# Kernel optimization log

Hardware: AMD Instinct MI355X
Metric: run time of the kernel (lower is better)

Reference implementation:

```python
import jax, jax.numpy as jnp
import numpy as np

D = 1024
H = 16
DK = D // H
TB = 64  # temporal_bias_dim
SCALE = DK ** -0.5


def setup_inputs() -> dict:
    key = jax.random.key(0)
    ks = jax.random.split(key, 12)
    B, S = 8, 512
    s = 0.02
    return {
        "x": jax.random.normal(ks[0], (B, S, D), jnp.float32),
        "padding_masks": jnp.ones((B, 1, 1, S), jnp.int32),
        "batch_temporal_mat": jax.random.uniform(ks[1], (B, S, S), jnp.float32) * 100.0,
        "wq": jax.random.normal(ks[2], (D, D), jnp.float32) * s,
        "bq": jnp.zeros((D,), jnp.float32),
        "wk": jax.random.normal(ks[3], (D, D), jnp.float32) * s,
        "bk": jnp.zeros((D,), jnp.float32),
        "wv": jax.random.normal(ks[4], (D, D), jnp.float32) * s,
        "bv": jnp.zeros((D,), jnp.float32),
        "w_proj": jax.random.normal(ks[5], (D, D), jnp.float32) * s,
        "b_proj": jnp.zeros((D,), jnp.float32),
        "w_tb1": jax.random.normal(ks[6], (1, TB), jnp.float32) * 0.5,
        "b_tb1": jnp.zeros((TB,), jnp.float32),
        "w_tb2": jax.random.normal(ks[7], (TB, 1), jnp.float32) * 0.5,
        "b_tb2": jnp.zeros((1,), jnp.float32),
    }


def reference(x, padding_masks, batch_temporal_mat, wq, bq, wk, bk, wv, bv,
              w_proj, b_proj, w_tb1, b_tb1, w_tb2, b_tb2):
    B, S, _ = x.shape

    def heads(w, b):
        return (x @ w + b).reshape(B, S, H, DK).transpose(0, 2, 1, 3)  # (B,H,S,DK)

    q, k, v = heads(wq, bq), heads(wk, bk), heads(wv, bv)
    scores = jnp.einsum("bhqd,bhkd->bhqk", q, k) * SCALE  # (B,H,S,S)

    # temporal bias: 1/log(e + t) -> Linear(1,64) -> leaky_relu(0.2) -> Linear(64,1)
    t = 1.0 / jnp.log(jnp.exp(jnp.float32(1.0)) + batch_temporal_mat)  # (B,S,S)
    h = t[..., None] * w_tb1[0] + b_tb1  # (B,S,S,TB)
    h = jnp.where(h >= 0, h, 0.2 * h)
    bias = (h @ w_tb2)[..., 0] + b_tb2[0]  # (B,S,S)
    scores = scores + bias[:, None, :, :]

    neg_inf = jnp.float32(-jnp.inf)
    scores = jnp.where(padding_masks == 0, neg_inf, scores)
    causal = jnp.triu(jnp.ones((S, S), bool), k=1)  # (S,S), add_cls=False
    scores = jnp.where(causal[None, None], neg_inf, scores)

    p_attn = jax.nn.softmax(scores, axis=-1)
    out = jnp.einsum("bhqk,bhkd->bhqd", p_attn, v)
    out = out.transpose(0, 2, 1, 3).reshape(B, S, D)
    out = out @ w_proj + b_proj
    return out
```

## Files before the change

### kernel.cpp

```cpp
#include <hip/hip_runtime.h>
#include <hip/hip_bf16.h>

#define B_  8
#define S_  512
#define D_  1024
#define H_  16
#define DK_ 64
#define TB_ 64
#define SCALE_ 0.125f

typedef __attribute__((ext_vector_type(8))) short          bh8;
typedef __attribute__((ext_vector_type(4))) float          f32x4;
typedef __attribute__((ext_vector_type(8))) unsigned short us8;

__device__ __forceinline__ unsigned short f2bf(float f) {
    unsigned u = __float_as_uint(f);
    unsigned r = 0x7fffu + ((u >> 16) & 1u);
    return (unsigned short)((u + r) >> 16);
}
__device__ __forceinline__ float bf2f(unsigned short u) {
    return __uint_as_float((unsigned)u << 16);
}

__device__ __forceinline__ void gl16(const unsigned short* g, unsigned short* l) {
    __builtin_amdgcn_global_load_lds(
        (const __attribute__((address_space(1))) void*)g,
        (__attribute__((address_space(3))) void*)l, 16, 0, 0);
}

__global__ __launch_bounds__(256)
void cvt_x_kernel(const float* __restrict__ in, unsigned short* __restrict__ out, int n8)
{
    int i = blockIdx.x * 256 + threadIdx.x;
    if (i >= n8) return;
    float4 a = *(const float4*)&in[(size_t)i * 8];
    float4 b = *(const float4*)&in[(size_t)i * 8 + 4];
    us8 o;
    o[0] = f2bf(a.x); o[1] = f2bf(a.y); o[2] = f2bf(a.z); o[3] = f2bf(a.w);
    o[4] = f2bf(b.x); o[5] = f2bf(b.y); o[6] = f2bf(b.z); o[7] = f2bf(b.w);
    *(us8*)&out[(size_t)i * 8] = o;
}

__global__ __launch_bounds__(256)
void cvt_wt4_kernel(const float* __restrict__ w0, const float* __restrict__ w1,
                    const float* __restrict__ w2, const float* __restrict__ w3,
                    unsigned short* __restrict__ o0, unsigned short* __restrict__ o1,
                    unsigned short* __restrict__ o2, unsigned short* __restrict__ o3)
{
    __shared__ float t[64][65];
    const int z = blockIdx.z;
    const float* W = (z == 0) ? w0 : (z == 1) ? w1 : (z == 2) ? w2 : w3;
    unsigned short* Wt = (z == 0) ? o0 : (z == 1) ? o1 : (z == 2) ? o2 : o3;
    const int bx = blockIdx.x, by = blockIdx.y;
    const int c  = threadIdx.x & 63;
    const int r0 = threadIdx.x >> 6;
    #pragma unroll
    for (int i = 0; i < 16; ++i) {
        int r = r0 + i * 4;
        t[r][c] = W[(size_t)(by * 64 + r) * 1024 + bx * 64 + c];
    }
    __syncthreads();
    #pragma unroll
    for (int i = 0; i < 16; ++i) {
        int r = r0 + i * 4;
        Wt[(size_t)(bx * 64 + r) * 1024 + by * 64 + c] = f2bf(t[c][r]);
    }
}

__global__ __launch_bounds__(256)
void gemm_qkv_kernel(const unsigned short* __restrict__ A,
                     const unsigned short* __restrict__ Wt,
                     const float* __restrict__ bq, const float* __restrict__ bk,
                     const float* __restrict__ bv,
                     unsigned short* __restrict__ qo,
                     unsigned short* __restrict__ ko,
                     unsigned short* __restrict__ vo)
{
    __shared__ unsigned short As[128 * 64];
    __shared__ unsigned short Bs[64 * 64];
    const int tid  = threadIdx.x;
    const int lane = tid & 63;
    const int wid  = tid >> 6;
    const int wr   = wid >> 1, wc = wid & 1;
    const int row0 = blockIdx.x * 128;
    const int col0 = blockIdx.y * 64;

    f32x4 acc[4][2] = {};

    const int fr = lane & 15;
    const int g  = lane >> 4;
    const int sr = lane >> 3;
    const int sc = ((lane & 7) ^ sr) * 8;

    for (int k0 = 0; k0 < 1024; k0 += 64) {
        #pragma unroll
        for (int i = 0; i < 4; ++i)
            gl16(&A [(size_t)(row0 + wid * 32 + i * 8 + sr) * 1024 + k0 + sc],
                 &As[(wid * 32 + i * 8) * 64]);
        #pragma unroll
        for (int i = 0; i < 2; ++i)
            gl16(&Wt[(size_t)(col0 + wid * 16 + i * 8 + sr) * 1024 + k0 + sc],
                 &Bs[(wid * 16 + i * 8) * 64]);
        __syncthreads();
        #pragma unroll
        for (int ks = 0; ks < 2; ++ks) {
            const int ch = (ks * 4 + g) ^ (fr & 7);
            bh8 af[4], bfr[2];
            #pragma unroll
            for (int r = 0; r < 4; ++r)
                af[r]  = *(const bh8*)&As[(wr * 64 + r * 16 + fr) * 64 + ch * 8];
            #pragma unroll
            for (int c = 0; c < 2; ++c)
                bfr[c] = *(const bh8*)&Bs[(wc * 32 + c * 16 + fr) * 64 + ch * 8];
            #pragma unroll
            for (int r = 0; r < 4; ++r)
                #pragma unroll
                for (int c = 0; c < 2; ++c)
                    acc[r][c] = __builtin_amdgcn_mfma_f32_16x16x32_bf16(
                        af[r], bfr[c], acc[r][c], 0, 0, 0);
        }
        __syncthreads();
    }

    const int nh = col0 >> 10;
    const float* bsel = (nh == 0) ? bq : (nh == 1) ? bk : bv;
    unsigned short* outp = (nh == 0) ? qo : (nh == 1) ? ko : vo;

    #pragma unroll
    for (int r = 0; r < 4; ++r) {
        #pragma unroll
        for (int c = 0; c < 2; ++c) {
            int n  = col0 + wc * 32 + c * 16 + fr;
            int nn = n & 1023;
            float bn = bsel[nn];
            int hh = nn >> 6, dd = nn & 63;
            #pragma unroll
            for (int j = 0; j < 4; ++j) {
                int m = row0 + wr * 64 + r * 16 + g * 4 + j;
                float o = acc[r][c][j] + bn;
                int bb = m >> 9, ss = m & 511;
                if (nh == 2)
                    outp[((size_t)((bb * H_ + hh) * DK_ + dd)) * S_ + ss] = f2bf(o);
                else
                    outp[((size_t)((bb * H_ + hh) * S_ + ss)) * DK_ + dd] = f2bf(o);
            }
        }
    }
}

#define GEMM_STAGE(buf, k0) do {                                         \
    gl16(Arow + (k0),            &As[buf][(w * 16    ) * 64]);           \
    gl16(Arow + (k0) + 8 * 1024, &As[buf][(w * 16 + 8) * 64]);           \
    gl16(Brow + (k0),            &Bs[buf][(w * 16    ) * 64]);           \
    gl16(Brow + (k0) + 8 * 1024, &Bs[buf][(w * 16 + 8) * 64]);           \
} while (0)

#define GEMM_COMPUTE(buf) do {                                           \
    _Pragma("unroll")                                                    \
    for (int ks = 0; ks < 2; ++ks) {                                     \
        const int ch = (ks * 4 + g) ^ (fr & 7);                          \
        bh8 af[2], bf[2];                                                \
        _Pragma("unroll")                                                \
        for (int r = 0; r < 2; ++r)                                      \
            af[r] = *(const bh8*)&As[buf][(wr * 32 + r * 16 + fr) * 64 + ch * 8]; \
        _Pragma("unroll")                                                \
        for (int c = 0; c < 2; ++c)                                      \
            bf[c] = *(const bh8*)&Bs[buf][(wc * 32 + c * 16 + fr) * 64 + ch * 8]; \
        _Pragma("unroll")                                                \
        for (int r = 0; r < 2; ++r)                                      \
            _Pragma("unroll")                                            \
            for (int c = 0; c < 2; ++c)                                  \
                acc[r][c] = __builtin_amdgcn_mfma_f32_16x16x32_bf16(     \
                    af[r], bf[c], acc[r][c], 0, 0, 0);                   \
    }                                                                    \
} while (0)

__global__ __launch_bounds__(256)
void gemm_proj_kernel(const unsigned short* __restrict__ A,
                      const unsigned short* __restrict__ Wt,
                      const float* __restrict__ bias,
                      float* __restrict__ C)
{
    __shared__ unsigned short As[2][64 * 64];
    __shared__ unsigned short Bs[2][64 * 64];
    const int tid  = threadIdx.x;
    const int lane = tid & 63;
    const int w    = tid >> 6;
    const int wr   = w >> 1, wc = w & 1;
    const int row0 = blockIdx.x * 64;
    const int col0 = blockIdx.y * 64;

    f32x4 acc[2][2] = {};
    const int fr = lane & 15;
    const int g  = lane >> 4;
    const int sr = lane >> 3;
    const int sc = ((lane & 7) ^ sr) * 8;

    const unsigned short* Arow = A  + (size_t)(row0 + w * 16 + sr) * 1024 + sc;
    const unsigned short* Brow = Wt + (size_t)(col0 + w * 16 + sr) * 1024 + sc;

    GEMM_STAGE(0, 0);
    __syncthreads();
    int cur = 0;
    #pragma unroll 1
    for (int t = 0; t < 15; ++t) {
        GEMM_STAGE(cur ^ 1, (t + 1) * 64);
        GEMM_COMPUTE(cur);
        __syncthreads();
        cur ^= 1;
    }
    GEMM_COMPUTE(cur);

    #pragma unroll
    for (int r = 0; r < 2; ++r) {
        #pragma unroll
        for (int c = 0; c < 2; ++c) {
            int n = col0 + wc * 32 + c * 16 + fr;
            float bn = bias[n];
            #pragma unroll
            for (int j = 0; j < 4; ++j) {
                int m = row0 + wr * 32 + r * 16 + g * 4 + j;
                C[(size_t)m * 1024 + n] = acc[r][c][j] + bn;
            }
        }
    }
}

__global__ __launch_bounds__(256)
void tbias_kernel(const float* __restrict__ tm, const int* __restrict__ pmask,
                  const float* __restrict__ w1, const float* __restrict__ b1,
                  const float* __restrict__ w2, const float* __restrict__ b2,
                  unsigned short* __restrict__ bias)
{
    __shared__ float sw1[TB_], sb1[TB_], sw2[TB_];
    if (threadIdx.x < TB_) {
        sw1[threadIdx.x] = w1[threadIdx.x];
        sb1[threadIdx.x] = b1[threadIdx.x];
        sw2[threadIdx.x] = w2[threadIdx.x];
    }
    __syncthreads();
    const float ec  = 2.7182818284590452f;
    const float b2v = b2[0];
    const int n = B_ * S_ * S_;
    for (int i = blockIdx.x * blockDim.x + threadIdx.x; i < n;
         i += gridDim.x * blockDim.x) {
        int bb = i >> 18;
        int jj = i & (S_ - 1);
        float t   = 1.0f / logf(ec + tm[i]);
        float acc = b2v;
        #pragma unroll
        for (int j = 0; j < TB_; ++j) {
            float h = fmaf(t, sw1[j], sb1[j]);
            h = (h >= 0.f) ? h : 0.2f * h;
            acc = fmaf(h, sw2[j], acc);
        }
        bias[i] = f2bf((pmask[bb * S_ + jj] == 0) ? -1e30f : acc);
    }
}

__global__ __launch_bounds__(256)
void attn_kernel(const unsigned short* __restrict__ q,
                 const unsigned short* __restrict__ k,
                 const unsigned short* __restrict__ vt,
                 const unsigned short* __restrict__ biasm,
                 unsigned short* __restrict__ outb)
{
    __shared__ unsigned short Kl[64][72];
    __shared__ unsigned short Vl[64][72];
    __shared__ unsigned short Pl[64][72];

    const int tid  = threadIdx.x;
    const int lane = tid & 63;
    const int w    = tid >> 6;
    const int lin = (blockIdx.x & 7) * 128 + (blockIdx.x >> 3);
    const int h   = lin & 15;
    const int qt  = (lin >> 4) & 7;
    const int b   = lin >> 7;
    const int q0  = qt * 64;

    const int l15 = lane & 15;
    const int g   = lane >> 4;

    const size_t hb  = (size_t)(b * H_ + h) * S_;
    const unsigned short* kbase  = k  + hb * DK_;
    const unsigned short* vtbase = vt + ((size_t)(b * H_ + h) * DK_) * S_;

    const int qrow_a = q0 + w * 16 + l15;
    bh8 aq0 = *(const bh8*)&q[(hb + qrow_a) * DK_ +      g * 8];
    bh8 aq1 = *(const bh8*)&q[(hb + qrow_a) * DK_ + 32 + g * 8];

    const int qd = q0 + w * 16 + g * 4;

    const int ur0 = tid >> 3,          uc0 = (tid & 7) * 8;
    const int ur1 = (tid + 256) >> 3,  uc1 = ((tid + 256) & 7) * 8;

    f32x4 acc_o[4] = {};
    float m_run[4] = { -1e30f, -1e30f, -1e30f, -1e30f };
    float l_run[4] = {};

    int4 kr0 = *(const int4*)&kbase [(size_t)ur0 * DK_ + uc0];
    int4 kr1 = *(const int4*)&kbase [(size_t)ur1 * DK_ + uc1];
    int4 vr0 = *(const int4*)&vtbase[(size_t)ur0 * S_ + uc0];
    int4 vr1 = *(const int4*)&vtbase[(size_t)ur1 * S_ + uc1];

    for (int kt = 0; kt <= qt; ++kt) {
        *(int4*)&Kl[ur0][uc0] = kr0;  *(int4*)&Kl[ur1][uc1] = kr1;
        *(int4*)&Vl[ur0][uc0] = vr0;  *(int4*)&Vl[ur1][uc1] = vr1;
        __syncthreads();

        if (kt < qt) {
            kr0 = *(const int4*)&kbase [(size_t)((kt+1) * 64 + ur0) * DK_ + uc0];
            kr1 = *(const int4*)&kbase [(size_t)((kt+1) * 64 + ur1) * DK_ + uc1];
            vr0 = *(const int4*)&vtbase[(size_t)ur0 * S_ + (kt+1) * 64 + uc0];
            vr1 = *(const int4*)&vtbase[(size_t)ur1 * S_ + (kt+1) * 64 + uc1];
        }

        f32x4 sc[4];
        #pragma unroll
        for (int c = 0; c < 4; ++c) {
            bh8 bk0 = *(const bh8*)&Kl[c * 16 + l15][     g * 8];
            bh8 bk1 = *(const bh8*)&Kl[c * 16 + l15][32 + g * 8];
            f32x4 z = {};
            z = __builtin_amdgcn_mfma_f32_16x16x32_bf16(aq0, bk0, z, 0, 0, 0);
            sc[c] = __builtin_amdgcn_mfma_f32_16x16x32_bf16(aq1, bk1, z, 0, 0, 0);
        }

        float sv[4][4];
        #pragma unroll
        for (int j = 0; j < 4; ++j) {
            const unsigned short* br = biasm + ((size_t)b * S_ + qd + j) * S_ + kt * 64;
            #pragma unroll
            for (int c = 0; c < 4; ++c)
                sv[c][j] = fmaf(sc[c][j], SCALE_, bf2f(br[c * 16 + l15]));
        }
        if (kt == qt) {
            #pragma unroll
            for (int c = 0; c < 4; ++c) {
                int kloc = c * 16 + l15;
                #pragma unroll
                for (int j = 0; j < 4; ++j)
                    if (kloc > w * 16 + g * 4 + j) sv[c][j] = -1e30f;
            }
        }

        #pragma unroll
        for (int j = 0; j < 4; ++j) {
            float mt = fmaxf(fmaxf(sv[0][j], sv[1][j]), fmaxf(sv[2][j], sv[3][j]));
            mt = fmaxf(mt, __shfl_xor(mt, 1));
            mt = fmaxf(mt, __shfl_xor(mt, 2));
            mt = fmaxf(mt, __shfl_xor(mt, 4));
            mt = fmaxf(mt, __shfl_xor(mt, 8));
            float m_new = fmaxf(m_run[j], mt);
            float resc  = __expf(m_run[j] - m_new);
            float psum  = 0.f;
            #pragma unroll
            for (int c = 0; c < 4; ++c) {
                float p = __expf(sv[c][j] - m_new);
                Pl[w * 16 + g * 4 + j][c * 16 + l15] = f2bf(p);
                psum += p;
            }
            psum += __shfl_xor(psum, 1);
            psum += __shfl_xor(psum, 2);
            psum += __shfl_xor(psum, 4);
            psum += __shfl_xor(psum, 8);
            l_run[j] = l_run[j] * resc + psum;
            m_run[j] = m_new;
            acc_o[0][j] *= resc; acc_o[1][j] *= resc;
            acc_o[2][j] *= resc; acc_o[3][j] *= resc;
        }

        asm volatile("s_waitcnt lgkmcnt(0)" ::: "memory");

        bh8 ap0 = *(const bh8*)&Pl[w * 16 + l15][     g * 8];
        bh8 ap1 = *(const bh8*)&Pl[w * 16 + l15][32 + g * 8];
        #pragma unroll
        for (int c2 = 0; c2 < 4; ++c2) {
            bh8 bv0 = *(const bh8*)&Vl[c2 * 16 + l15][     g * 8];
            bh8 bv1 = *(const bh8*)&Vl[c2 * 16 + l15][32 + g * 8];
            acc_o[c2] = __builtin_amdgcn_mfma_f32_16x16x32_bf16(ap0, bv0, acc_o[c2], 0, 0, 0);
            acc_o[c2] = __builtin_amdgcn_mfma_f32_16x16x32_bf16(ap1, bv1, acc_o[c2], 0, 0, 0);
        }
        __syncthreads();
    }

    #pragma unroll
    for (int j = 0; j < 4; ++j) {
        float linv = 1.f / l_run[j];
        #pragma unroll
        for (int c2 = 0; c2 < 4; ++c2)
            outb[((size_t)(b * S_ + qd + j)) * D_ + h * DK_ + c2 * 16 + l15] =
                f2bf(acc_o[c2][j] * linv);
    }
}

extern "C" void kernel_launch(void* const* d_in, const int* in_sizes, int n_in,
                              void* d_out, int out_size, void* d_ws, size_t ws_size,
                              hipStream_t stream)
{
    const float* x     = (const float*)d_in[0];
    const int*   pm    = (const int*)  d_in[1];
    const float* tm    = (const float*)d_in[2];
    const float* wq    = (const float*)d_in[3];
    const float* bq    = (const float*)d_in[4];
    const float* wk    = (const float*)d_in[5];
    const float* bk    = (const float*)d_in[6];
    const float* wv    = (const float*)d_in[7];
    const float* bv    = (const float*)d_in[8];
    const float* wp    = (const float*)d_in[9];
    const float* bp    = (const float*)d_in[10];
    const float* w_tb1 = (const float*)d_in[11];
    const float* b_tb1 = (const float*)d_in[12];
    const float* w_tb2 = (const float*)d_in[13];
    const float* b_tb2 = (const float*)d_in[14];

    char* wsb = (char*)d_ws;
    const size_t MB = 1u << 20;
    unsigned short* xb   = (unsigned short*)wsb;
    unsigned short* wqkv = (unsigned short*)(wsb + 8  * MB);
    unsigned short* wtp  = (unsigned short*)(wsb + 14 * MB);
    unsigned short* qw   = (unsigned short*)(wsb + 16 * MB);
    unsigned short* kw   = (unsigned short*)(wsb + 24 * MB);
    unsigned short* vtw  = (unsigned short*)(wsb + 32 * MB);
    unsigned short* bw   = (unsigned short*)(wsb + 40 * MB);

    cvt_x_kernel<<<2048, 256, 0, stream>>>(x, xb, 524288);
    dim3 gw(16, 16, 4);
    cvt_wt4_kernel<<<gw, 256, 0, stream>>>(wq, wk, wv, wp,
                                           wqkv, wqkv + 1048576, wqkv + 2097152, wtp);

    dim3 gqkv(32, 48);
    gemm_qkv_kernel<<<gqkv, 256, 0, stream>>>(xb, wqkv, bq, bk, bv, qw, kw, vtw);

    tbias_kernel<<<2048, 256, 0, stream>>>(tm, pm, w_tb1, b_tb1, w_tb2, b_tb2, bw);

    attn_kernel<<<1024, 256, 0, stream>>>(qw, kw, vtw, bw, xb );

    dim3 gp(64, 16);
    gemm_proj_kernel<<<gp, 256, 0, stream>>>(xb, wtp, bp, (float*)d_out);
}
```

Baseline: 224.6 us.

## Merge prep kernels into one launch and drop register prefetch in attention

Folds the x conversion, weight transpose/convert and temporal-bias computation into a single block-partitioned prep kernel, removing two launches and letting the independent preprocessing stages run concurrently. Separately, the attention kernel drops its register-staged prefetch of the next K/V tile and loads each tile directly into LDS between two barriers. This trims register pressure and launch overhead but loses the overlap of global loads with the previous tile's compute.

```diff
diff --git a/kernel.cpp b/kernel.cpp
--- a/kernel.cpp
+++ b/kernel.cpp
@@ -29,41 +29,74 @@
 }
 
 __global__ __launch_bounds__(256)
-void cvt_x_kernel(const float* __restrict__ in, unsigned short* __restrict__ out, int n8)
+void prep_kernel(const float* __restrict__ x, unsigned short* __restrict__ xb,
+                 const float* __restrict__ w0, const float* __restrict__ w1w,
+                 const float* __restrict__ w2w, const float* __restrict__ w3w,
+                 unsigned short* __restrict__ o0, unsigned short* __restrict__ o1,
+                 unsigned short* __restrict__ o2, unsigned short* __restrict__ o3,
+                 const float* __restrict__ tm, const int* __restrict__ pmask,
+                 const float* __restrict__ tw1, const float* __restrict__ tb1,
+                 const float* __restrict__ tw2, const float* __restrict__ tb2,
+                 unsigned short* __restrict__ biasb)
 {
-    int i = blockIdx.x * 256 + threadIdx.x;
-    if (i >= n8) return;
-    float4 a = *(const float4*)&in[(size_t)i * 8];
-    float4 b = *(const float4*)&in[(size_t)i * 8 + 4];
-    us8 o;
-    o[0] = f2bf(a.x); o[1] = f2bf(a.y); o[2] = f2bf(a.z); o[3] = f2bf(a.w);
-    o[4] = f2bf(b.x); o[5] = f2bf(b.y); o[6] = f2bf(b.z); o[7] = f2bf(b.w);
-    *(us8*)&out[(size_t)i * 8] = o;
-}
-
-__global__ __launch_bounds__(256)
-void cvt_wt4_kernel(const float* __restrict__ w0, const float* __restrict__ w1,
-                    const float* __restrict__ w2, const float* __restrict__ w3,
-                    unsigned short* __restrict__ o0, unsigned short* __restrict__ o1,
-                    unsigned short* __restrict__ o2, unsigned short* __restrict__ o3)
-{
-    __shared__ float t[64][65];
-    const int z = blockIdx.z;
-    const float* W = (z == 0) ? w0 : (z == 1) ? w1 : (z == 2) ? w2 : w3;
-    unsigned short* Wt = (z == 0) ? o0 : (z == 1) ? o1 : (z == 2) ? o2 : o3;
-    const int bx = blockIdx.x, by = blockIdx.y;
-    const int c  = threadIdx.x & 63;
-    const int r0 = threadIdx.x >> 6;
-    #pragma unroll
-    for (int i = 0; i < 16; ++i) {
-        int r = r0 + i * 4;
-        t[r][c] = W[(size_t)(by * 64 + r) * 1024 + bx * 64 + c];
-    }
-    __syncthreads();
-    #pragma unroll
-    for (int i = 0; i < 16; ++i) {
-        int r = r0 + i * 4;
-        Wt[(size_t)(bx * 64 + r) * 1024 + by * 64 + c] = f2bf(t[c][r]);
+    __shared__ float smem[64 * 65];
+    const int bid = blockIdx.x;
+    const int tid = threadIdx.x;
+
+    if (bid < 2048) {
+        int i = bid * 256 + tid;
+        float4 a = *(const float4*)&x[(size_t)i * 8];
+        float4 b = *(const float4*)&x[(size_t)i * 8 + 4];
+        us8 o;
+        o[0] = f2bf(a.x); o[1] = f2bf(a.y); o[2] = f2bf(a.z); o[3] = f2bf(a.w);
+        o[4] = f2bf(b.x); o[5] = f2bf(b.y); o[6] = f2bf(b.z); o[7] = f2bf(b.w);
+        *(us8*)&xb[(size_t)i * 8] = o;
+    } else if (bid < 3072) {
+        int idx = bid - 2048;
+        int z = idx >> 8, local = idx & 255;
+        int bx = local & 15, by = local >> 4;
+        const float* W = (z == 0) ? w0 : (z == 1) ? w1w : (z == 2) ? w2w : w3w;
+        unsigned short* Wt = (z == 0) ? o0 : (z == 1) ? o1 : (z == 2) ? o2 : o3;
+        float (*t)[65] = (float(*)[65])smem;
+        const int c  = tid & 63;
+        const int r0 = tid >> 6;
+        #pragma unroll
+        for (int i = 0; i < 16; ++i) {
+            int r = r0 + i * 4;
+            t[r][c] = W[(size_t)(by * 64 + r) * 1024 + bx * 64 + c];
+        }
+        __syncthreads();
+        #pragma unroll
+        for (int i = 0; i < 16; ++i) {
+            int r = r0 + i * 4;
+            Wt[(size_t)(bx * 64 + r) * 1024 + by * 64 + c] = f2bf(t[c][r]);
+        }
+    } else {
+        float* sw1 = smem;
+        float* sb1 = smem + 64;
+        float* sw2 = smem + 128;
+        if (tid < TB_) {
+            sw1[tid] = tw1[tid];
+            sb1[tid] = tb1[tid];
+            sw2[tid] = tw2[tid];
+        }
+        __syncthreads();
+        const float ec  = 2.7182818284590452f;
+        const float b2v = tb2[0];
+        const int n = B_ * S_ * S_;
+        for (int i = (bid - 3072) * 256 + tid; i < n; i += 2048 * 256) {
+            int bb = i >> 18;
+            int jj = i & (S_ - 1);
+            float t   = 1.0f / logf(ec + tm[i]);
+            float acc = b2v;
+            #pragma unroll
+            for (int j = 0; j < TB_; ++j) {
+                float h = fmaf(t, sw1[j], sb1[j]);
+                h = (h >= 0.f) ? h : 0.2f * h;
+                acc = fmaf(h, sw2[j], acc);
+            }
+            biasb[i] = f2bf((pmask[bb * S_ + jj] == 0) ? -1e30f : acc);
+        }
     }
 }
 
@@ -227,38 +260,6 @@
 }
 
 __global__ __launch_bounds__(256)
-void tbias_kernel(const float* __restrict__ tm, const int* __restrict__ pmask,
-                  const float* __restrict__ w1, const float* __restrict__ b1,
-                  const float* __restrict__ w2, const float* __restrict__ b2,
-                  unsigned short* __restrict__ bias)
-{
-    __shared__ float sw1[TB_], sb1[TB_], sw2[TB_];
-    if (threadIdx.x < TB_) {
-        sw1[threadIdx.x] = w1[threadIdx.x];
-        sb1[threadIdx.x] = b1[threadIdx.x];
-        sw2[threadIdx.x] = w2[threadIdx.x];
-    }
-    __syncthreads();
-    const float ec  = 2.7182818284590452f;
-    const float b2v = b2[0];
-    const int n = B_ * S_ * S_;
-    for (int i = blockIdx.x * blockDim.x + threadIdx.x; i < n;
-         i += gridDim.x * blockDim.x) {
-        int bb = i >> 18;
-        int jj = i & (S_ - 1);
-        float t   = 1.0f / logf(ec + tm[i]);
-        float acc = b2v;
-        #pragma unroll
-        for (int j = 0; j < TB_; ++j) {
-            float h = fmaf(t, sw1[j], sb1[j]);
-            h = (h >= 0.f) ? h : 0.2f * h;
-            acc = fmaf(h, sw2[j], acc);
-        }
-        bias[i] = f2bf((pmask[bb * S_ + jj] == 0) ? -1e30f : acc);
-    }
-}
-
-__global__ __launch_bounds__(256)
 void attn_kernel(const unsigned short* __restrict__ q,
                  const unsigned short* __restrict__ k,
                  const unsigned short* __restrict__ vt,
@@ -291,29 +292,21 @@
 
     const int qd = q0 + w * 16 + g * 4;
 
-    const int ur0 = tid >> 3,          uc0 = (tid & 7) * 8;
-    const int ur1 = (tid + 256) >> 3,  uc1 = ((tid + 256) & 7) * 8;
-
     f32x4 acc_o[4] = {};
     float m_run[4] = { -1e30f, -1e30f, -1e30f, -1e30f };
     float l_run[4] = {};
 
-    int4 kr0 = *(const int4*)&kbase [(size_t)ur0 * DK_ + uc0];
-    int4 kr1 = *(const int4*)&kbase [(size_t)ur1 * DK_ + uc1];
-    int4 vr0 = *(const int4*)&vtbase[(size_t)ur0 * S_ + uc0];
-    int4 vr1 = *(const int4*)&vtbase[(size_t)ur1 * S_ + uc1];
-
     for (int kt = 0; kt <= qt; ++kt) {
-        *(int4*)&Kl[ur0][uc0] = kr0;  *(int4*)&Kl[ur1][uc1] = kr1;
-        *(int4*)&Vl[ur0][uc0] = vr0;  *(int4*)&Vl[ur1][uc1] = vr1;
-        __syncthreads();
-
-        if (kt < qt) {
-            kr0 = *(const int4*)&kbase [(size_t)((kt+1) * 64 + ur0) * DK_ + uc0];
-            kr1 = *(const int4*)&kbase [(size_t)((kt+1) * 64 + ur1) * DK_ + uc1];
-            vr0 = *(const int4*)&vtbase[(size_t)ur0 * S_ + (kt+1) * 64 + uc0];
-            vr1 = *(const int4*)&vtbase[(size_t)ur1 * S_ + (kt+1) * 64 + uc1];
-        }
+        __syncthreads();
+        #pragma unroll
+        for (int s = 0; s < 2; ++s) {
+            int u  = tid + s * 256;
+            int r  = u >> 3;
+            int c8 = (u & 7) * 8;
+            *(int4*)&Kl[r][c8] = *(const int4*)&kbase [(size_t)(kt * 64 + r) * DK_ + c8];
+            *(int4*)&Vl[r][c8] = *(const int4*)&vtbase[(size_t)r * S_ + kt * 64 + c8];
+        }
+        __syncthreads();
 
         f32x4 sc[4];
         #pragma unroll
@@ -380,7 +373,6 @@
             acc_o[c2] = __builtin_amdgcn_mfma_f32_16x16x32_bf16(ap0, bv0, acc_o[c2], 0, 0, 0);
             acc_o[c2] = __builtin_amdgcn_mfma_f32_16x16x32_bf16(ap1, bv1, acc_o[c2], 0, 0, 0);
         }
-        __syncthreads();
     }
 
     #pragma unroll
@@ -423,16 +415,14 @@
     unsigned short* vtw  = (unsigned short*)(wsb + 32 * MB);
     unsigned short* bw   = (unsigned short*)(wsb + 40 * MB);
 
-    cvt_x_kernel<<<2048, 256, 0, stream>>>(x, xb, 524288);
-    dim3 gw(16, 16, 4);
-    cvt_wt4_kernel<<<gw, 256, 0, stream>>>(wq, wk, wv, wp,
-                                           wqkv, wqkv + 1048576, wqkv + 2097152, wtp);
+    prep_kernel<<<5120, 256, 0, stream>>>(
+        x, xb, wq, wk, wv, wp,
+        wqkv, wqkv + 1048576, wqkv + 2097152, wtp,
+        tm, pm, w_tb1, b_tb1, w_tb2, b_tb2, bw);
 
     dim3 gqkv(32, 48);
     gemm_qkv_kernel<<<gqkv, 256, 0, stream>>>(xb, wqkv, bq, bk, bv, qw, kw, vtw);
 
-    tbias_kernel<<<2048, 256, 0, stream>>>(tm, pm, w_tb1, b_tb1, w_tb2, b_tb2, bw);
-
     attn_kernel<<<1024, 256, 0, stream>>>(qw, kw, vtw, bw, xb );
 
     dim3 gp(64, 16);
```

Measured after the change: 239.7 us. +6.7%, slower.
